# Performance work log

Measured on AMD Instinct MI355X. Metric: run time of the kernel, lower is better.

The kernel has to match this reference:

```python
import jax, jax.numpy as jnp
import numpy as np

B, S, D = 4, 2048, 1024
KEY_DIM, VALUE_DIM = 1024, 1024
BETA = 1.0 / np.sqrt(D)  # beta defaults to 1/sqrt(input dim), per build()


def setup_inputs() -> dict:
    key = jax.random.key(0)
    ks = jax.random.split(key, 9)
    inv = 1.0 / np.sqrt(D)
    return {
        "query": jax.random.normal(ks[0], (B, S, D), dtype=jnp.float32),
        "key": jax.random.normal(ks[1], (B, S, D), dtype=jnp.float32),
        "value": jax.random.normal(ks[2], (B, S, D), dtype=jnp.float32),
        "Wq": jax.random.normal(ks[3], (D, KEY_DIM), dtype=jnp.float32) * inv,
        "bq": jnp.zeros((KEY_DIM,), dtype=jnp.float32),
        "Wk": jax.random.normal(ks[4], (D, KEY_DIM), dtype=jnp.float32) * inv,
        "bk": jnp.zeros((KEY_DIM,), dtype=jnp.float32),
        "Wv": jax.random.normal(ks[5], (D, VALUE_DIM), dtype=jnp.float32) * inv,
        "bv": jnp.zeros((VALUE_DIM,), dtype=jnp.float32),
    }


def reference(query, key, value, Wq, bq, Wk, bk, Wv, bv):
    # Dense projections
    q = query @ Wq + bq          # [B, S, key_dim]
    k = key @ Wk + bk            # [B, S, key_dim]
    v = value @ Wv + bv          # [B, S, value_dim]
    # Scaled dot-product attention (beta applied AFTER matmul, as in source)
    scores = jnp.einsum("bik,bjk->bij", q, k)  # [B, S, S]
    A = jax.nn.softmax(BETA * scores, axis=-1)
    return jnp.einsum("bij,bjk->bik", A, v)    # [B, S, value_dim]
```

## Files before the change

### kernel.cpp

```cpp
#include <hip/hip_runtime.h>


typedef __bf16 bf16x8 __attribute__((ext_vector_type(8)));
typedef float f32x4 __attribute__((ext_vector_type(4)));

#define MIB ((size_t)1 << 20)

__device__ __forceinline__ unsigned short f2b(float f) {
  unsigned int u = __float_as_uint(f);
  return (unsigned short)((u + 0x7FFFu + ((u >> 16) & 1u)) >> 16);
}

__device__ __forceinline__ void async16(const void* g, void* l) {
  __builtin_amdgcn_global_load_lds(
      (const __attribute__((address_space(1))) unsigned int*)g,
      (__attribute__((address_space(3))) unsigned int*)l, 16, 0, 0);
}

__device__ __forceinline__ unsigned ldsoff(const void* p) {
  return (unsigned)(size_t)(const __attribute__((address_space(3))) char*)p;
}

__device__ __forceinline__ bf16x8 ds_read16(unsigned off) {
  bf16x8 r;
  asm volatile("ds_read_b128 %0, %1" : "=v"(r) : "v"(off));
  return r;
}

template <int TN>
__device__ __forceinline__ void stage_tile(
    const unsigned short* __restrict__ A, const unsigned short* __restrict__ Bt,
    unsigned short* dst, int K, int kb, int tid) {
#pragma unroll
  for (int i = 0; i < 4; ++i) {
    const int e = i * 256 + tid;
    const int r = e >> 3;
    const int cg = (e & 7) ^ (r & 7);
    async16(A + (size_t)r * K + kb + cg * 8, dst + e * 8);
  }
#pragma unroll
  for (int i = 0; i < TN / 32; ++i) {
    const int e = i * 256 + tid;
    const int r = e >> 3;
    const int cg = (e & 7) ^ (r & 7);
    async16(Bt + (size_t)r * K + kb + cg * 8, dst + 128 * 64 + e * 8);
  }
}

template <int TN, bool SWAP>
__device__ __forceinline__ void gemm_loop(
    const unsigned short* __restrict__ A, const unsigned short* __restrict__ Bt,
    unsigned short* lds, int K, int m0, int n0, f32x4 (&acc)[4][TN / 32]) {
  constexpr int NI = TN / 32;
  constexpr unsigned BUFB = (128 + TN) * 64 * 2;
  const int tid = threadIdx.x;
  const int lane = tid & 63;
  const int wave = tid >> 6;
  const int wm = (wave >> 1) * 64;
  const int wn = (wave & 1) * (TN / 2);
  const int fr = lane & 15;
  const int q = lane >> 4;
  const int NT = K >> 6;

  const unsigned short* Ab = A + (size_t)m0 * K;
  const unsigned short* Bb = Bt + (size_t)n0 * K;
  const unsigned LB = ldsoff(lds);

  unsigned oa[4][2], ob[NI][2];
#pragma unroll
  for (int mi = 0; mi < 4; ++mi) {
    const int R = wm + mi * 16 + fr;
#pragma unroll
    for (int ks = 0; ks < 2; ++ks) {
      const int kc = ks * 4 + q;
      oa[mi][ks] = (unsigned)((R * 64 + ((kc ^ (R & 7)) << 3)) * 2);
    }
  }
#pragma unroll
  for (int ni = 0; ni < NI; ++ni) {
    const int R = wn + ni * 16 + fr;
#pragma unroll
    for (int ks = 0; ks < 2; ++ks) {
      const int kc = ks * 4 + q;
      ob[ni][ks] =
          (unsigned)(128 * 64 * 2 + (R * 64 + ((kc ^ (R & 7)) << 3)) * 2);
    }
  }

  stage_tile<TN>(Ab, Bb, lds, K, 0, tid);
  __syncthreads();

  for (int t = 0; t < NT; ++t) {
    const unsigned boff = LB + (unsigned)(t & 1) * BUFB;
    if (t + 1 < NT)
      stage_tile<TN>(Ab, Bb, lds + ((t + 1) & 1) * (BUFB / 2), K,
                     (t + 1) << 6, tid);

    bf16x8 av[2][4], bv[2][NI];
#pragma unroll
    for (int ks = 0; ks < 2; ++ks)
#pragma unroll
      for (int mi = 0; mi < 4; ++mi) av[ks][mi] = ds_read16(boff + oa[mi][ks]);
#pragma unroll
    for (int ks = 0; ks < 2; ++ks)
#pragma unroll
      for (int ni = 0; ni < NI; ++ni) bv[ks][ni] = ds_read16(boff + ob[ni][ks]);

    asm volatile("s_waitcnt lgkmcnt(0)");
    __builtin_amdgcn_sched_barrier(0);

#pragma unroll
    for (int ks = 0; ks < 2; ++ks)
#pragma unroll
      for (int mi = 0; mi < 4; ++mi)
#pragma unroll
        for (int ni = 0; ni < NI; ++ni)
          acc[mi][ni] = SWAP ? __builtin_amdgcn_mfma_f32_16x16x32_bf16(
                                   bv[ks][ni], av[ks][mi], acc[mi][ni], 0, 0, 0)
                             : __builtin_amdgcn_mfma_f32_16x16x32_bf16(
                                   av[ks][mi], bv[ks][ni], acc[mi][ni], 0, 0, 0);

    __syncthreads();
  }
}

struct ProjArgs {
  const unsigned short* A[3];
  const unsigned short* Bt[3];
  unsigned short* C[3];
  const float* bias[3];
};

__global__ __launch_bounds__(256) void proj_qk(ProjArgs p) {
  __shared__ __align__(16) unsigned short lds[2 * 256 * 64];
  const int z = blockIdx.z;
  const int m0 = blockIdx.x * 128;
  const int n0 = blockIdx.y * 128;

  f32x4 acc[4][4] = {};
  gemm_loop<128, true>(p.A[z], p.Bt[z], lds, 1024, m0, n0, acc);

  const int lane = threadIdx.x & 63;
  const int wave = threadIdx.x >> 6;
  const int wm = (wave >> 1) * 64;
  const int wn = (wave & 1) * 64;
  const int fr = lane & 15;
  const int q4 = (lane >> 4) * 4;
  const float* bias = p.bias[z];
  unsigned short* C = p.C[z];

#pragma unroll
  for (int mi = 0; mi < 4; ++mi) {
    const int m = m0 + wm + mi * 16 + fr;
#pragma unroll
    for (int ni = 0; ni < 4; ++ni) {
      const int nb = n0 + wn + ni * 16 + q4;
      const float4 bb = *(const float4*)&bias[nb];
      ushort4 o = make_ushort4(
          f2b(acc[mi][ni][0] + bb.x), f2b(acc[mi][ni][1] + bb.y),
          f2b(acc[mi][ni][2] + bb.z), f2b(acc[mi][ni][3] + bb.w));
      *(ushort4*)&C[(size_t)m * 1024 + nb] = o;
    }
  }
}

__global__ __launch_bounds__(256) void proj_v(ProjArgs p) {
  __shared__ __align__(16) unsigned short lds[2 * 256 * 64];
  const int m0 = blockIdx.x * 128;
  const int n0 = blockIdx.y * 128;

  f32x4 acc[4][4] = {};
  gemm_loop<128, false>(p.A[2], p.Bt[2], lds, 1024, m0, n0, acc);

  const int lane = threadIdx.x & 63;
  const int wave = threadIdx.x >> 6;
  const int wm = (wave >> 1) * 64;
  const int wn = (wave & 1) * 64;
  const int fr = lane & 15;
  const int q4 = (lane >> 4) * 4;
  const float* bias = p.bias[2];

  unsigned short* C = p.C[2] + (size_t)(m0 >> 11) * (2048 * 1024);
#pragma unroll
  for (int mi = 0; mi < 4; ++mi) {
#pragma unroll
    for (int ni = 0; ni < 4; ++ni) {
      const int col = n0 + wn + ni * 16 + fr;
      const float bb = bias[col];
      const int rowb = (m0 + wm + mi * 16 + q4) & 2047;
      ushort4 o =
          make_ushort4(f2b(acc[mi][ni][0] + bb), f2b(acc[mi][ni][1] + bb),
                       f2b(acc[mi][ni][2] + bb), f2b(acc[mi][ni][3] + bb));
      *(ushort4*)&C[(size_t)col * 2048 + rowb] = o;
    }
  }
}

__global__ __launch_bounds__(256) void gemm_f32(
    const unsigned short* __restrict__ A, const unsigned short* __restrict__ Bt,
    float* __restrict__ C, int K, int ldc, long long sA, long long sB,
    long long sC) {
  __shared__ __align__(16) unsigned short lds[2 * 256 * 64];
  const int bz = blockIdx.z;
  A += (long long)bz * sA;
  Bt += (long long)bz * sB;
  C += (long long)bz * sC;
  const int m0 = blockIdx.x * 128;
  const int n0 = blockIdx.y * 128;

  f32x4 acc[4][4] = {};
  gemm_loop<128, true>(A, Bt, lds, K, m0, n0, acc);

  const int lane = threadIdx.x & 63;
  const int wave = threadIdx.x >> 6;
  const int wm = (wave >> 1) * 64;
  const int wn = (wave & 1) * 64;
  const int fr = lane & 15;
  const int q4 = (lane >> 4) * 4;
#pragma unroll
  for (int mi = 0; mi < 4; ++mi) {
    const int m = m0 + wm + mi * 16 + fr;
#pragma unroll
    for (int ni = 0; ni < 4; ++ni) {
      const int nb = n0 + wn + ni * 16 + q4;
      *(f32x4*)&C[(size_t)m * ldc + nb] = acc[mi][ni];
    }
  }
}

__global__ __launch_bounds__(256) void prep(
    const float4* __restrict__ xq, const float4* __restrict__ xk,
    const float4* __restrict__ xv, ushort4* __restrict__ oq,
    ushort4* __restrict__ ok, ushort4* __restrict__ ov,
    const float* __restrict__ w0, const float* __restrict__ w1,
    const float* __restrict__ w2, unsigned short* __restrict__ t0,
    unsigned short* __restrict__ t1, unsigned short* __restrict__ t2) {
  __shared__ float tl[32][33];
  const int bid = blockIdx.x;
  if (bid < 24576) {
    const int ten = bid >> 13;
    const int i = (bid & 8191) * 256 + threadIdx.x;
    const float4* src = (ten == 0) ? xq : (ten == 1) ? xk : xv;
    ushort4* dst = (ten == 0) ? oq : (ten == 1) ? ok : ov;
    float4 x = src[i];
    dst[i] = make_ushort4(f2b(x.x), f2b(x.y), f2b(x.z), f2b(x.w));
  } else {
    const int t = bid - 24576;
    const int z = t >> 10;
    const int rem = t & 1023;
    const int n0 = (rem & 31) * 32, k0 = (rem >> 5) * 32;
    const float* W = (z == 0) ? w0 : (z == 1) ? w1 : w2;
    unsigned short* WT = (z == 0) ? t0 : (z == 1) ? t1 : t2;
    const int tx = threadIdx.x & 31, ty = threadIdx.x >> 5;
#pragma unroll
    for (int i = 0; i < 32; i += 8)
      tl[ty + i][tx] = W[(size_t)(k0 + ty + i) * 1024 + (n0 + tx)];
    __syncthreads();
#pragma unroll
    for (int i = 0; i < 32; i += 8)
      WT[(size_t)(n0 + ty + i) * 1024 + (k0 + tx)] = f2b(tl[tx][ty + i]);
  }
}

__global__ __launch_bounds__(256) void softmax_rows(const float* __restrict__ S,
                                                    unsigned short* __restrict__ P) {
  const int cols = 2048;
  const size_t row = blockIdx.x;
  const float4* srow = (const float4*)(S + row * cols);
  const int tid = threadIdx.x;
  const int lane = tid & 63;
  const int wave = tid >> 6;

  float4 a = srow[tid];
  float4 b = srow[tid + 256];

  float mx = fmaxf(fmaxf(fmaxf(a.x, a.y), fmaxf(a.z, a.w)),
                   fmaxf(fmaxf(b.x, b.y), fmaxf(b.z, b.w)));
#pragma unroll
  for (int o = 1; o < 64; o <<= 1) mx = fmaxf(mx, __shfl_xor(mx, o));

  __shared__ float red[8];
  if (lane == 0) red[wave] = mx;
  __syncthreads();
  mx = fmaxf(fmaxf(red[0], red[1]), fmaxf(red[2], red[3]));

  const float c = 0.03125f * 1.4426950408889634f;
  float4 pa, pb;
  pa.x = exp2f((a.x - mx) * c); pa.y = exp2f((a.y - mx) * c);
  pa.z = exp2f((a.z - mx) * c); pa.w = exp2f((a.w - mx) * c);
  pb.x = exp2f((b.x - mx) * c); pb.y = exp2f((b.y - mx) * c);
  pb.z = exp2f((b.z - mx) * c); pb.w = exp2f((b.w - mx) * c);

  float sum = pa.x + pa.y + pa.z + pa.w + pb.x + pb.y + pb.z + pb.w;
#pragma unroll
  for (int o = 1; o < 64; o <<= 1) sum += __shfl_xor(sum, o);
  if (lane == 0) red[4 + wave] = sum;
  __syncthreads();
  sum = red[4] + red[5] + red[6] + red[7];

  const float inv = 1.0f / sum;
  ushort4* prow = (ushort4*)(P + row * cols);
  prow[tid] = make_ushort4(f2b(pa.x * inv), f2b(pa.y * inv), f2b(pa.z * inv),
                           f2b(pa.w * inv));
  prow[tid + 256] = make_ushort4(f2b(pb.x * inv), f2b(pb.y * inv),
                                 f2b(pb.z * inv), f2b(pb.w * inv));
}

extern "C" void kernel_launch(void* const* d_in, const int* in_sizes, int n_in,
                              void* d_out, int out_size, void* d_ws, size_t ws_size,
                              hipStream_t stream) {
  const float* query = (const float*)d_in[0];
  const float* key_ = (const float*)d_in[1];
  const float* value = (const float*)d_in[2];
  const float* Wq = (const float*)d_in[3];
  const float* bq = (const float*)d_in[4];
  const float* Wk = (const float*)d_in[5];
  const float* bk = (const float*)d_in[6];
  const float* Wv = (const float*)d_in[7];
  const float* bv = (const float*)d_in[8];
  float* out = (float*)d_out;

  char* ws = (char*)d_ws;
  unsigned short* WqT = (unsigned short*)ws;
  unsigned short* WkT = WqT + (size_t)1024 * 1024;
  unsigned short* WvT = WkT + (size_t)1024 * 1024;
  unsigned short* Xq = (unsigned short*)(ws + 6 * MIB);
  unsigned short* Xk = Xq + (size_t)8192 * 1024;
  unsigned short* Xv = Xk + (size_t)8192 * 1024;
  unsigned short* qb = (unsigned short*)(ws + 54 * MIB);
  unsigned short* kb = (unsigned short*)(ws + 70 * MIB);
  unsigned short* vT = (unsigned short*)(ws + 86 * MIB);
  float* sc = (float*)(ws + 102 * MIB);
  unsigned short* P = (unsigned short*)(ws + 6 * MIB);

  prep<<<dim3(27648), 256, 0, stream>>>(
      (const float4*)query, (const float4*)key_, (const float4*)value,
      (ushort4*)Xq, (ushort4*)Xk, (ushort4*)Xv, Wq, Wk, Wv, WqT, WkT, WvT);

  ProjArgs pa;
  pa.A[0] = Xq;  pa.A[1] = Xk;  pa.A[2] = Xv;
  pa.Bt[0] = WqT; pa.Bt[1] = WkT; pa.Bt[2] = WvT;
  pa.C[0] = qb;  pa.C[1] = kb;  pa.C[2] = vT;
  pa.bias[0] = bq; pa.bias[1] = bk; pa.bias[2] = bv;

  proj_qk<<<dim3(64, 8, 2), 256, 0, stream>>>(pa);
  proj_v<<<dim3(64, 8, 1), 256, 0, stream>>>(pa);

  gemm_f32<<<dim3(16, 16, 4), 256, 0, stream>>>(
      qb, kb, sc, 1024, 2048, 2048LL * 1024, 2048LL * 1024, 2048LL * 2048);

  softmax_rows<<<8192, 256, 0, stream>>>(sc, P);

  gemm_f32<<<dim3(16, 8, 4), 256, 0, stream>>>(
      P, vT, out, 2048, 1024, 2048LL * 2048, 1024LL * 2048, 2048LL * 1024);
}
```

Measured before the change: 319.7 us.

## Use 256x256 tiles with 512-thread blocks for Q/K projection and score GEMM

```diff
diff --git a/kernel.cpp b/kernel.cpp
--- a/kernel.cpp
+++ b/kernel.cpp
@@ -25,6 +25,154 @@
   bf16x8 r;
   asm volatile("ds_read_b128 %0, %1" : "=v"(r) : "v"(off));
   return r;
+}
+
+__device__ __forceinline__ void stage256(
+    const unsigned short* __restrict__ Ab, const unsigned short* __restrict__ Bb,
+    unsigned short* dst, int K, int kb, int tid) {
+#pragma unroll
+  for (int i = 0; i < 4; ++i) {
+    const int e = i * 512 + tid;
+    const int r = e >> 3;
+    const int cg = (e & 7) ^ (r & 7);
+    async16(Ab + (size_t)r * K + kb + cg * 8, dst + e * 8);
+  }
+#pragma unroll
+  for (int i = 0; i < 4; ++i) {
+    const int e = i * 512 + tid;
+    const int r = e >> 3;
+    const int cg = (e & 7) ^ (r & 7);
+    async16(Bb + (size_t)r * K + kb + cg * 8, dst + 16384 + e * 8);
+  }
+}
+
+__device__ __forceinline__ void gemm256(
+    const unsigned short* __restrict__ A, const unsigned short* __restrict__ Bt,
+    unsigned short* lds, int K, int m0, int n0, f32x4 (&acc)[8][4]) {
+  const int tid = threadIdx.x;
+  const int lane = tid & 63;
+  const int wave = tid >> 6;
+  const int wm = (wave >> 2) * 128;
+  const int wn = (wave & 3) * 64;
+  const int fr = lane & 15;
+  const int q = lane >> 4;
+  const int NT = K >> 6;
+
+  const unsigned short* Ab = A + (size_t)m0 * K;
+  const unsigned short* Bb = Bt + (size_t)n0 * K;
+  const unsigned LB = ldsoff(lds);
+
+  unsigned oa[8], ob[4];
+#pragma unroll
+  for (int mi = 0; mi < 8; ++mi) {
+    const int R = wm + mi * 16 + fr;
+    oa[mi] = (unsigned)((R * 64 + ((q ^ (R & 7)) << 3)) * 2);
+  }
+#pragma unroll
+  for (int ni = 0; ni < 4; ++ni) {
+    const int R = wn + ni * 16 + fr;
+    ob[ni] = (unsigned)(32768 + (R * 64 + ((q ^ (R & 7)) << 3)) * 2);
+  }
+
+  stage256(Ab, Bb, lds, K, 0, tid);
+  __syncthreads();
+
+  for (int t = 0; t < NT; ++t) {
+    const unsigned boff = LB + (unsigned)(t & 1) * 65536;
+    if (t + 1 < NT)
+      stage256(Ab, Bb, lds + ((t + 1) & 1) * 32768, K, (t + 1) << 6, tid);
+
+#pragma unroll
+    for (int ks = 0; ks < 2; ++ks) {
+      const unsigned kx = ks ? 64u : 0u;
+      bf16x8 av[8], bv[4];
+#pragma unroll
+      for (int mi = 0; mi < 8; ++mi) av[mi] = ds_read16((boff + oa[mi]) ^ kx);
+#pragma unroll
+      for (int ni = 0; ni < 4; ++ni) bv[ni] = ds_read16((boff + ob[ni]) ^ kx);
+
+      asm volatile("s_waitcnt lgkmcnt(0)");
+      __builtin_amdgcn_sched_barrier(0);
+
+#pragma unroll
+      for (int mi = 0; mi < 8; ++mi)
+#pragma unroll
+        for (int ni = 0; ni < 4; ++ni)
+          acc[mi][ni] = __builtin_amdgcn_mfma_f32_16x16x32_bf16(
+              bv[ni], av[mi], acc[mi][ni], 0, 0, 0);
+    }
+    __syncthreads();
+  }
+}
+
+struct ProjArgs {
+  const unsigned short* A[3];
+  const unsigned short* Bt[3];
+  unsigned short* C[3];
+  const float* bias[3];
+};
+
+__global__ __launch_bounds__(512, 2) void proj_qk256(ProjArgs p) {
+  __shared__ __align__(16) unsigned short lds[65536];
+  const int z = blockIdx.z;
+  const int m0 = blockIdx.x * 256;
+  const int n0 = blockIdx.y * 256;
+
+  f32x4 acc[8][4] = {};
+  gemm256(p.A[z], p.Bt[z], lds, 1024, m0, n0, acc);
+
+  const int lane = threadIdx.x & 63;
+  const int wave = threadIdx.x >> 6;
+  const int wm = (wave >> 2) * 128;
+  const int wn = (wave & 3) * 64;
+  const int fr = lane & 15;
+  const int q4 = (lane >> 4) * 4;
+  const float* bias = p.bias[z];
+  unsigned short* C = p.C[z];
+
+#pragma unroll
+  for (int mi = 0; mi < 8; ++mi) {
+    const int m = m0 + wm + mi * 16 + fr;
+#pragma unroll
+    for (int ni = 0; ni < 4; ++ni) {
+      const int nb = n0 + wn + ni * 16 + q4;
+      const float4 bb = *(const float4*)&bias[nb];
+      ushort4 o = make_ushort4(
+          f2b(acc[mi][ni][0] + bb.x), f2b(acc[mi][ni][1] + bb.y),
+          f2b(acc[mi][ni][2] + bb.z), f2b(acc[mi][ni][3] + bb.w));
+      *(ushort4*)&C[(size_t)m * 1024 + nb] = o;
+    }
+  }
+}
+
+__global__ __launch_bounds__(512, 2) void score256(
+    const unsigned short* __restrict__ qb, const unsigned short* __restrict__ kb,
+    float* __restrict__ sc) {
+  __shared__ __align__(16) unsigned short lds[65536];
+  const int bz = blockIdx.z;
+  const int m0 = blockIdx.x * 256;
+  const int n0 = blockIdx.y * 256;
+
+  f32x4 acc[8][4] = {};
+  gemm256(qb + (size_t)bz * (2048 * 1024), kb + (size_t)bz * (2048 * 1024),
+          lds, 1024, m0, n0, acc);
+
+  float* C = sc + (size_t)bz * (2048 * 2048);
+  const int lane = threadIdx.x & 63;
+  const int wave = threadIdx.x >> 6;
+  const int wm = (wave >> 2) * 128;
+  const int wn = (wave & 3) * 64;
+  const int fr = lane & 15;
+  const int q4 = (lane >> 4) * 4;
+#pragma unroll
+  for (int mi = 0; mi < 8; ++mi) {
+    const int m = m0 + wm + mi * 16 + fr;
+#pragma unroll
+    for (int ni = 0; ni < 4; ++ni) {
+      const int nb = n0 + wn + ni * 16 + q4;
+      *(f32x4*)&C[(size_t)m * 2048 + nb] = acc[mi][ni];
+    }
+  }
 }
 
 template <int TN>
@@ -121,46 +269,6 @@
                                    av[ks][mi], bv[ks][ni], acc[mi][ni], 0, 0, 0);
 
     __syncthreads();
-  }
-}
-
-struct ProjArgs {
-  const unsigned short* A[3];
-  const unsigned short* Bt[3];
-  unsigned short* C[3];
-  const float* bias[3];
-};
-
-__global__ __launch_bounds__(256) void proj_qk(ProjArgs p) {
-  __shared__ __align__(16) unsigned short lds[2 * 256 * 64];
-  const int z = blockIdx.z;
-  const int m0 = blockIdx.x * 128;
-  const int n0 = blockIdx.y * 128;
-
-  f32x4 acc[4][4] = {};
-  gemm_loop<128, true>(p.A[z], p.Bt[z], lds, 1024, m0, n0, acc);
-
-  const int lane = threadIdx.x & 63;
-  const int wave = threadIdx.x >> 6;
-  const int wm = (wave >> 1) * 64;
-  const int wn = (wave & 1) * 64;
-  const int fr = lane & 15;
-  const int q4 = (lane >> 4) * 4;
-  const float* bias = p.bias[z];
-  unsigned short* C = p.C[z];
-
-#pragma unroll
-  for (int mi = 0; mi < 4; ++mi) {
-    const int m = m0 + wm + mi * 16 + fr;
-#pragma unroll
-    for (int ni = 0; ni < 4; ++ni) {
-      const int nb = n0 + wn + ni * 16 + q4;
-      const float4 bb = *(const float4*)&bias[nb];
-      ushort4 o = make_ushort4(
-          f2b(acc[mi][ni][0] + bb.x), f2b(acc[mi][ni][1] + bb.y),
-          f2b(acc[mi][ni][2] + bb.z), f2b(acc[mi][ni][3] + bb.w));
-      *(ushort4*)&C[(size_t)m * 1024 + nb] = o;
-    }
   }
 }
 
@@ -343,11 +451,10 @@
   pa.C[0] = qb;  pa.C[1] = kb;  pa.C[2] = vT;
   pa.bias[0] = bq; pa.bias[1] = bk; pa.bias[2] = bv;
 
-  proj_qk<<<dim3(64, 8, 2), 256, 0, stream>>>(pa);
+  proj_qk256<<<dim3(32, 4, 2), 512, 0, stream>>>(pa);
   proj_v<<<dim3(64, 8, 1), 256, 0, stream>>>(pa);
 
-  gemm_f32<<<dim3(16, 16, 4), 256, 0, stream>>>(
-      qb, kb, sc, 1024, 2048, 2048LL * 1024, 2048LL * 1024, 2048LL * 2048);
+  score256<<<dim3(8, 8, 4), 512, 0, stream>>>(qb, kb, sc);
 
   softmax_rows<<<8192, 256, 0, stream>>>(sc, P);
 
```

Result: faster. 305.8 us (-4.3%).
